# Kernel optimization log

Measured on AMD Instinct MI355X. Metric: run time of the kernel, lower is better.

The kernel has to match this reference:

```python
import jax, jax.numpy as jnp
import numpy as np
import math

B, L, D_MODEL = 4, 2048, 512
EXPAND, D_STATE, D_CONV = 6, 8, 3
D_INNER = EXPAND * D_MODEL            # 3072
DT_RANK = math.ceil(D_MODEL / 16)     # 32
NH = 8
HF = D_MODEL // NH                    # 64


def setup_inputs() -> dict:
    key = jax.random.key(0)
    ks = jax.random.split(key, 16)
    n = lambda k, sh, s=0.02: jax.random.normal(k, sh, dtype=jnp.float32) * s
    return {
        "x": jax.random.normal(ks[0], (B, L, D_MODEL), dtype=jnp.float32),
        "norm_w": jnp.ones((D_MODEL,), jnp.float32),
        "in_proj_w": n(ks[1], (2 * D_INNER, D_MODEL)),
        "conv_w": n(ks[2], (D_INNER, 1, D_CONV), 0.2),
        "conv_b": jnp.zeros((D_INNER,), jnp.float32),
        "x_proj_w": n(ks[3], (DT_RANK + 2 * D_STATE, D_INNER)),
        "dt_head_w": n(ks[4], (D_INNER, DT_RANK)),
        "dt_head_b": jnp.zeros((D_INNER,), jnp.float32),
        "D": jnp.ones((D_INNER,), jnp.float32),
        "reduce_w": n(ks[5], (D_MODEL, D_INNER)),
        "q_net_w": n(ks[6], (D_MODEL, D_MODEL)),
        "gain_q_w": n(ks[7], (D_MODEL, D_MODEL)),
        "gain_k_w": n(ks[8], (D_MODEL, D_MODEL)),
        "alpha": jnp.ones((1,), jnp.float32),
        "beta": jnp.zeros((1,), jnp.float32),
        "qkv_w": n(ks[9], (3 * D_MODEL + NH, D_MODEL)),
        "qkv_b": jnp.zeros((3 * D_MODEL + NH,), jnp.float32),
        "ttt_lr_bias": jnp.zeros((NH,), jnp.float32),
        "W1": n(ks[10], (NH, HF, HF)),
        "b1": jnp.zeros((NH, HF), jnp.float32),
        "token_idx": 1.0 / jnp.arange(1, L + 1, dtype=jnp.float32),
        "token_idx_bias": jnp.zeros((L,), jnp.float32),
        "ttt_ln_w": jnp.ones((NH, HF), jnp.float32),
        "ttt_ln_b": jnp.zeros((NH, HF), jnp.float32),
        "post_norm_w": jnp.ones((D_MODEL,), jnp.float32),
        "post_norm_b": jnp.zeros((D_MODEL,), jnp.float32),
        "wo_w": n(ks[11], (D_MODEL, D_MODEL)),
        "wo_b": jnp.zeros((D_MODEL,), jnp.float32),
    }


def _rmsnorm(x, w, eps=1e-5):
    return x * jax.lax.rsqrt(jnp.mean(x * x, axis=-1, keepdims=True) + eps) * w


def _layernorm(x, w, b, eps=1e-5):
    mu = x.mean(-1, keepdims=True)
    xh = (x - mu) * jax.lax.rsqrt(x.var(-1, keepdims=True) + eps)
    return xh * w + b


def _longhorn_scan(x, z, dt, k, q, dt_b, D):
    # x,z,dt: [B,L,di]; k,q: [B,L,ds].  Online Longhorn recurrence (matches step()).
    def step(s, t):
        x_t, z_t, dt_t, k_t, q_t = t
        dt_t = jax.nn.sigmoid(dt_t + dt_b)
        dt_t = dt_t / (1.0 + dt_t * jnp.sum(k_t * k_t, -1, keepdims=True))
        dB = dt_t[:, :, None] * k_t[:, None, :]                  # [B,di,ds]
        s = s * (1.0 - dB * k_t[:, None, :]) + x_t[:, :, None] * dB
        y_t = jnp.einsum('bdn,bn->bd', s, q_t) + D * x_t
        return s, y_t * jax.nn.silu(z_t)

    s0 = jnp.zeros((x.shape[0], x.shape[2], k.shape[2]), x.dtype)
    xs = tuple(jnp.moveaxis(a, 1, 0) for a in (x, z, dt, k, q))
    _, ys = jax.lax.scan(step, s0, xs)
    return jnp.moveaxis(ys, 0, 1)                                # [B,L,di]


def _ttt(h, qkv_w, qkv_b, ttt_lr_bias, W1, b1, token_idx, token_idx_bias,
         ln_w, ln_b, pn_w, pn_b, wo_w, wo_b, lr_mult=1.0):
    Bh, N, d = h.shape
    proj = h @ qkv_w.T + qkv_b                                   # [B,N,3d+NH]
    XQK, XV, XGate, lr = (proj[..., :d], proj[..., d:2 * d],
                          proj[..., 2 * d:3 * d], proj[..., 3 * d:])

    def heads(a):  # [B,N,d] -> [B*NH,N,HF]
        return a.reshape(Bh, N, NH, HF).transpose(0, 2, 1, 3).reshape(Bh * NH, N, HF)

    XQ = heads(XQK)            # XQ == XK in the source
    XVh = heads(XV)
    ttt_lr = jax.nn.sigmoid(lr + ttt_lr_bias) * lr_mult          # [B,N,NH]
    ttt_lr = jnp.swapaxes(ttt_lr, 0, 1).reshape(N, Bh * NH, 1)   # [N,B*NH,1]
    tok = jnp.maximum(token_idx + token_idx_bias, 0.0)           # [N]

    W1c = jnp.broadcast_to(W1[None], (Bh, NH, HF, HF)).reshape(Bh * NH, HF, HF)
    b1c = jnp.broadcast_to(b1[None], (Bh, NH, HF)).reshape(Bh * NH, HF)
    lnw = jnp.broadcast_to(ln_w[None], (Bh, NH, HF)).reshape(Bh * NH, HF)
    lnb = jnp.broadcast_to(ln_b[None], (Bh, NH, HF)).reshape(Bh * NH, HF)
    eps = 1e-6
    HFf = jnp.float32(HF)

    def step(carry, t):
        W, bb = carry
        xk, xv, lr_t, tok_t = t
        Z1 = jnp.einsum('bf,bfg->bg', xk, W) + bb
        mu = Z1.mean(-1, keepdims=True)
        std = jnp.sqrt(Z1.var(-1, keepdims=True) + eps)
        xh = (Z1 - mu) / std
        # grad of ||LN(Z1) - (XV - XK)||^2 wrt Z1 (ln_fused_l2_bwd)
        go = (lnw * xh + lnb) - (xv - xk)
        gxh = go * lnw
        grad = (HFf * gxh - gxh.sum(-1, keepdims=True)
                - xh * (gxh * xh).sum(-1, keepdims=True)) / (HFf * std)
        eta = lr_t * tok_t                                       # [B*NH,1]
        W = W - eta[:, :, None] * (xk[:, :, None] * grad[:, None, :])
        bb = bb - eta * grad
        Z1q = jnp.einsum('bf,bfg->bg', xk, W) + bb
        mu2 = Z1q.mean(-1, keepdims=True)
        std2 = jnp.sqrt(Z1q.var(-1, keepdims=True) + eps)
        out_t = xk + lnw * (Z1q - mu2) / std2 + lnb
        return (W, bb), out_t

    xs = (jnp.moveaxis(XQ, 1, 0), jnp.moveaxis(XVh, 1, 0), ttt_lr, tok)
    _, ys = jax.lax.scan(step, (W1c, b1c), xs)                   # [N,B*NH,HF]
    xqw = ys.reshape(N, Bh, NH, HF).transpose(1, 0, 2, 3).reshape(Bh, N, d)
    normed = _layernorm(xqw, pn_w, pn_b)
    gated = jax.nn.gelu(XGate, approximate=True) * normed
    return gated @ wo_w.T + wo_b


def reference(x, norm_w, in_proj_w, conv_w, conv_b, x_proj_w, dt_head_w, dt_head_b,
              D, reduce_w, q_net_w, gain_q_w, gain_k_w, alpha, beta,
              qkv_w, qkv_b, ttt_lr_bias, W1, b1, token_idx, token_idx_bias,
              ttt_ln_w, ttt_ln_b, post_norm_w, post_norm_b, wo_w, wo_b):
    residual = x                                   # residual=None in forward
    xn = _rmsnorm(residual, norm_w)
    # ---- Longhorn block ----
    xz = xn @ in_proj_w.T                          # [B,L,2*di]
    xx, z = jnp.split(xz, 2, axis=-1)
    xc = jnp.swapaxes(xx, 1, 2)                    # [B,di,L]
    xc = jax.lax.conv_general_dilated(
        xc, conv_w, (1,), [(D_CONV - 1, 0)],       # causal depthwise conv
        dimension_numbers=('NCH', 'OIH', 'NCH'), feature_group_count=D_INNER)
    xc = jax.nn.silu(xc + conv_b[None, :, None])
    xb = jnp.swapaxes(xc, 1, 2)                    # [B,L,di]
    x_dbl = xb @ x_proj_w.T
    dt = x_dbl[..., :DT_RANK] @ dt_head_w.T        # [B,L,di] (bias added in scan)
    k = x_dbl[..., DT_RANK:DT_RANK + D_STATE]
    q = x_dbl[..., DT_RANK + D_STATE:]
    y = _longhorn_scan(xb, z, dt, k, q, dt_head_b, D)   # h_hidden, [B,L,di]
    # (out_proj output is discarded by PreCoBlock, so not computed)
    h_red = y @ reduce_w.T                          # [B,L,d]
    # ---- TTT corrective branch ----
    c_hidden = _ttt(h_red, qkv_w, qkv_b, ttt_lr_bias, W1, b1, token_idx,
                    token_idx_bias, ttt_ln_w, ttt_ln_b, post_norm_w, post_norm_b,
                    wo_w, wo_b, lr_mult=1.0)
    z_long = h_red @ q_net_w.T
    z_ttt = c_hidden @ q_net_w.T
    gq = h_red @ gain_q_w.T
    gk = h_red @ gain_k_w.T
    # score = mean_i (gq_i . gk_j)/sqrt(d) == (mean_i gq_i) . gk_j / sqrt(d)
    score = jnp.einsum('bd,bld->bl', gq.mean(axis=1), gk) / jnp.sqrt(jnp.float32(D_MODEL))
    gain = jnp.minimum(jax.nn.sigmoid(alpha * score + beta), 0.55)[..., None]
    out = z_long + gain * (z_ttt - z_long)
    return (out, residual, gain)
```

## Files before the change

kernel.cpp:

```cpp
#include <hip/hip_runtime.h>
#include <hip/hip_bf16.h>
#include <cstdint>
#include <cstddef>

#define L_SEQ 2048
#define BATCH 4
#define DM    512
#define DI    3072
#define NROWS (BATCH * L_SEQ)
#define PROJW 1544
#define CTILE 16
#define BDI   (BATCH * DI)
#define SB    64
#define NSB   (L_SEQ / SB)
#define CHT   16
#define LCH   128
#define NLCH  (L_SEQ / LCH)

using bf16 = __hip_bfloat16;

typedef __attribute__((ext_vector_type(8))) short short8v;
typedef __attribute__((ext_vector_type(4))) float f32x4;


__device__ __forceinline__ float sigmoidf_(float x) { return 1.f / (1.f + __expf(-x)); }
__device__ __forceinline__ float us2f(unsigned int u) {
    union { unsigned int i; float f; } c; c.i = u << 16; return c.f;
}
__device__ __forceinline__ bf16  f2b(float f) { return __float2bfloat16(f); }
__device__ __forceinline__ float b2f(bf16 v)  { return __bfloat162float(v); }
__device__ __forceinline__ void st1(float* p, float v) { *p = v; }
__device__ __forceinline__ void st1(bf16* p, float v)  { *p = f2b(v); }

template <int CTRL>
__device__ __forceinline__ float dppadd_(float x) {
    int s = __builtin_amdgcn_update_dpp(0, __builtin_bit_cast(int, x), CTRL, 0xF, 0xF, true);
    return x + __builtin_bit_cast(float, s);
}
__device__ __forceinline__ float wave_sum_u(float x) {
    x = dppadd_<0x111>(x);
    x = dppadd_<0x112>(x);
    x = dppadd_<0x114>(x);
    x = dppadd_<0x118>(x);
    x = dppadd_<0x142>(x);
    x = dppadd_<0x143>(x);
    return __builtin_bit_cast(float,
        __builtin_amdgcn_readlane(__builtin_bit_cast(int, x), 63));
}

__global__ __launch_bounds__(256) void copy4_k(const float4* __restrict__ in,
                                               float4* __restrict__ out, int n) {
    int i = blockIdx.x * 256 + threadIdx.x;
    if (i < n) out[i] = in[i];
}

__global__ __launch_bounds__(256) void cvt_k(const float* __restrict__ in,
                                             bf16* __restrict__ out, int n4) {
    int i = blockIdx.x * 256 + threadIdx.x;
    if (i >= n4) return;
    float4 v = ((const float4*)in)[i];
    out[4 * i + 0] = f2b(v.x);
    out[4 * i + 1] = f2b(v.y);
    out[4 * i + 2] = f2b(v.z);
    out[4 * i + 3] = f2b(v.w);
}

__global__ __launch_bounds__(256) void rmsnorm_k(const float* __restrict__ x,
                                                 const float* __restrict__ w,
                                                 bf16* __restrict__ xn) {
    int r = blockIdx.x, tid = threadIdx.x;
    const float* row = x + (size_t)r * DM;
    float v0 = row[tid], v1 = row[tid + 256];
    float q = v0 * v0 + v1 * v1;
#pragma unroll
    for (int off = 32; off; off >>= 1) q += __shfl_xor(q, off);
    __shared__ float sm[4];
    if ((tid & 63) == 0) sm[tid >> 6] = q;
    __syncthreads();
    q = sm[0] + sm[1] + sm[2] + sm[3];
    float scale = rsqrtf(q * (1.f / 512.f) + 1e-5f);
    bf16* orow = xn + (size_t)r * DM;
    orow[tid]       = f2b(v0 * scale * w[tid]);
    orow[tid + 256] = f2b(v1 * scale * w[tid + 256]);
}

template <int BIAS, typename TC>
__global__ __launch_bounds__(256) void gemm_mfma(const bf16* __restrict__ A, int lda,
                                                 const bf16* __restrict__ Wb, int ldw,
                                                 const float* __restrict__ bias,
                                                 TC* __restrict__ C, int ldc,
                                                 int N, int K) {
    __shared__ __align__(16) bf16 As[128 * 48];
    __shared__ __align__(16) bf16 Ws[128 * 48];
    const int tid = threadIdx.x;
    const int lane = tid & 63;
    const int widx = tid >> 6;
    const int bm = blockIdx.x * 128;
    const int bn = blockIdx.y * 128;
    const int wr = (widx >> 1) * 64;
    const int wc = (widx & 1) * 64;

    f32x4 acc[4][4];
#pragma unroll
    for (int i = 0; i < 4; ++i)
#pragma unroll
        for (int j = 0; j < 4; ++j) acc[i][j] = (f32x4){0.f, 0.f, 0.f, 0.f};

    const int r0 = tid >> 2;
    const int c0 = tid & 3;
    const int frow = lane & 15;
    const int fk = (lane >> 4) * 8;

    int n0 = bn + r0;       if (n0 > N - 1) n0 = N - 1;
    int n1 = bn + r0 + 64;  if (n1 > N - 1) n1 = N - 1;
    const bf16* pa0 = A + (size_t)(bm + r0) * lda + c0 * 8;
    const bf16* pa1 = A + (size_t)(bm + r0 + 64) * lda + c0 * 8;
    const bf16* pb0 = Wb + (size_t)n0 * ldw + c0 * 8;
    const bf16* pb1 = Wb + (size_t)n1 * ldw + c0 * 8;

    for (int k0 = 0; k0 < K; k0 += 32) {
        short8v a0 = *(const short8v*)(pa0 + k0);
        short8v a1 = *(const short8v*)(pa1 + k0);
        short8v b0 = *(const short8v*)(pb0 + k0);
        short8v b1 = *(const short8v*)(pb1 + k0);
        __syncthreads();
        *(short8v*)&As[r0 * 48 + c0 * 8] = a0;
        *(short8v*)&As[(r0 + 64) * 48 + c0 * 8] = a1;
        *(short8v*)&Ws[r0 * 48 + c0 * 8] = b0;
        *(short8v*)&Ws[(r0 + 64) * 48 + c0 * 8] = b1;
        __syncthreads();
        short8v af[4], bg[4];
#pragma unroll
        for (int mi = 0; mi < 4; ++mi)
            af[mi] = *(const short8v*)&As[(wr + mi * 16 + frow) * 48 + fk];
#pragma unroll
        for (int ni = 0; ni < 4; ++ni)
            bg[ni] = *(const short8v*)&Ws[(wc + ni * 16 + frow) * 48 + fk];
#pragma unroll
        for (int mi = 0; mi < 4; ++mi)
#pragma unroll
            for (int ni = 0; ni < 4; ++ni)
                acc[mi][ni] = __builtin_amdgcn_mfma_f32_16x16x32_bf16(
                    af[mi], bg[ni], acc[mi][ni], 0, 0, 0);
    }

#pragma unroll
    for (int ni = 0; ni < 4; ++ni) {
        int col = bn + wc + ni * 16 + (lane & 15);
        if (col < N) {
            float bz = BIAS ? bias[col] : 0.f;
#pragma unroll
            for (int mi = 0; mi < 4; ++mi) {
                int rbase = bm + wr + mi * 16 + (lane >> 4) * 4;
#pragma unroll
                for (int r = 0; r < 4; ++r) {
                    float v = acc[mi][ni][r] + bz;
                    st1(&C[(size_t)(rbase + r) * ldc + col], v);
                }
            }
        }
    }
}

__global__ __launch_bounds__(256) void conv_boundary_k(const bf16* __restrict__ x,
                                                       bf16* __restrict__ side) {
    int idx = blockIdx.x * 256 + threadIdx.x;
    const int total = (L_SEQ / CTILE - 1) * 2 * BDI;
    if (idx >= total) return;
    int col = idx % BDI;
    int rr = idx / BDI;
    int tile = (rr >> 1) + 1;
    int r = rr & 1;
    int b = col / DI, d = col % DI;
    int l = tile * CTILE - 2 + r;
    side[idx] = x[((size_t)b * L_SEQ + l) * DI + d];
}

__global__ __launch_bounds__(256) void conv_tile_k(bf16* __restrict__ x,
                                                   const bf16* __restrict__ side,
                                                   const float* __restrict__ cw,
                                                   const float* __restrict__ cb) {
    int idx = blockIdx.x * 256 + threadIdx.x;
    const int total = (L_SEQ / CTILE) * BDI;
    if (idx >= total) return;
    int col = idx % BDI;
    int tile = idx / BDI;
    int b = col / DI, d = col % DI;
    float w0 = cw[3 * d], w1 = cw[3 * d + 1], w2 = cw[3 * d + 2], bias = cb[d];
    size_t base = ((size_t)b * L_SEQ + tile * CTILE) * DI + d;
    float xm2, xm1;
    if (tile == 0) { xm2 = 0.f; xm1 = 0.f; }
    else {
        const bf16* sp = side + ((size_t)(tile - 1) * 2) * BDI + col;
        xm2 = b2f(sp[0]);
        xm1 = b2f(sp[BDI]);
    }
    float cur = b2f(x[base]);
#pragma unroll
    for (int i = 0; i < CTILE; ++i) {
        float nxt = (i + 1 < CTILE) ? b2f(x[base + (size_t)(i + 1) * DI]) : 0.f;
        float a = bias + w0 * xm2 + w1 * xm1 + w2 * cur;
        x[base + (size_t)i * DI] = f2b(a * sigmoidf_(a));
        xm2 = xm1; xm1 = cur; cur = nxt;
    }
}


__global__ __launch_bounds__(256) void longhorn_p1(const bf16* __restrict__ xb,
                                                   const float* __restrict__ xdbl,
                                                   const float* __restrict__ dtw,
                                                   const float* __restrict__ dtb_v,
                                                   float* __restrict__ pq) {
    int idx = blockIdx.x * 256 + threadIdx.x;
    int ch = idx / BDI;
    int col = idx % BDI;
    int b = col / DI, d = col % DI;
    float w32[32];
#pragma unroll
    for (int i = 0; i < 32; ++i) w32[i] = dtw[d * 32 + i];
    float dtb = dtb_v[d];
    float P[8] = {1.f, 1.f, 1.f, 1.f, 1.f, 1.f, 1.f, 1.f};
    float Q[8] = {0.f, 0.f, 0.f, 0.f, 0.f, 0.f, 0.f, 0.f};
    size_t rbase = ((size_t)b * L_SEQ + ch * LCH) * DI + d;
    const float* xdb = xdbl + ((size_t)b * L_SEQ + ch * LCH) * 48;

    float xv = b2f(xb[rbase]);
    for (int t = 0; t < LCH; ++t) {
        float x_c = xv;
        if (t + 1 < LCH) xv = b2f(xb[rbase + (size_t)(t + 1) * DI]);
        const float* row = xdb + (size_t)t * 48;
        float dt_c = 0.f;
#pragma unroll
        for (int i = 0; i < 32; i += 4) {
            float4 r4 = *(const float4*)(row + i);
            dt_c = fmaf(r4.x, w32[i + 0], dt_c);
            dt_c = fmaf(r4.y, w32[i + 1], dt_c);
            dt_c = fmaf(r4.z, w32[i + 2], dt_c);
            dt_c = fmaf(r4.w, w32[i + 3], dt_c);
        }
        float kq[8];
#pragma unroll
        for (int i = 0; i < 8; i += 4) *(float4*)&kq[i] = *(const float4*)(row + 32 + i);
        float sig = sigmoidf_(dt_c + dtb);
        float ksq = 0.f;
#pragma unroll
        for (int n = 0; n < 8; ++n) ksq = fmaf(kq[n], kq[n], ksq);
        float dts = sig / (1.f + sig * ksq);
#pragma unroll
        for (int n = 0; n < 8; ++n) {
            float dB = dts * kq[n];
            float a = 1.f - dB * kq[n];
            P[n] *= a;
            Q[n] = fmaf(Q[n], a, x_c * dB);
        }
    }
    float* o = pq + (size_t)idx * 16;
#pragma unroll
    for (int n = 0; n < 8; n += 4) {
        *(float4*)(o + n)     = make_float4(P[n], P[n + 1], P[n + 2], P[n + 3]);
        *(float4*)(o + 8 + n) = make_float4(Q[n], Q[n + 1], Q[n + 2], Q[n + 3]);
    }
}

__global__ __launch_bounds__(256) void longhorn_p2(float* __restrict__ pq) {
    int col = blockIdx.x * 256 + threadIdx.x;
    float s[8] = {0.f, 0.f, 0.f, 0.f, 0.f, 0.f, 0.f, 0.f};
    for (int c = 0; c < NLCH; ++c) {
        float* base = pq + ((size_t)c * BDI + col) * 16;
        float P[8], Q[8];
#pragma unroll
        for (int n = 0; n < 8; n += 4) {
            *(float4*)&P[n] = *(const float4*)(base + n);
            *(float4*)&Q[n] = *(const float4*)(base + 8 + n);
        }
#pragma unroll
        for (int n = 0; n < 8; n += 4)
            *(float4*)(base + n) = make_float4(s[n], s[n + 1], s[n + 2], s[n + 3]);
#pragma unroll
        for (int n = 0; n < 8; ++n) s[n] = fmaf(P[n], s[n], Q[n]);
    }
}

__global__ __launch_bounds__(256) void longhorn_p3(bf16* __restrict__ xb_y,
                                                   const bf16* __restrict__ z,
                                                   const float* __restrict__ xdbl,
                                                   const float* __restrict__ dtw,
                                                   const float* __restrict__ dtb_v,
                                                   const float* __restrict__ Dv,
                                                   const float* __restrict__ pq) {
    int idx = blockIdx.x * 256 + threadIdx.x;
    int ch = idx / BDI;
    int col = idx % BDI;
    int b = col / DI, d = col % DI;
    float w32[32];
#pragma unroll
    for (int i = 0; i < 32; ++i) w32[i] = dtw[d * 32 + i];
    float dtb = dtb_v[d], Dd = Dv[d];
    float s[8];
    {
        const float* base = pq + (size_t)idx * 16;
#pragma unroll
        for (int n = 0; n < 8; n += 4) *(float4*)&s[n] = *(const float4*)(base + n);
    }
    size_t rbase = ((size_t)b * L_SEQ + ch * LCH) * DI + d;
    const float* xdb = xdbl + ((size_t)b * L_SEQ + ch * LCH) * 48;

    float xv = b2f(xb_y[rbase]);
    float zv = b2f(z[rbase]);
    for (int t = 0; t < LCH; ++t) {
        float x_c = xv, z_c = zv;
        if (t + 1 < LCH) {
            size_t nidx = rbase + (size_t)(t + 1) * DI;
            xv = b2f(xb_y[nidx]);
            zv = b2f(z[nidx]);
        }
        const float* row = xdb + (size_t)t * 48;
        float dt_c = 0.f;
#pragma unroll
        for (int i = 0; i < 32; i += 4) {
            float4 r4 = *(const float4*)(row + i);
            dt_c = fmaf(r4.x, w32[i + 0], dt_c);
            dt_c = fmaf(r4.y, w32[i + 1], dt_c);
            dt_c = fmaf(r4.z, w32[i + 2], dt_c);
            dt_c = fmaf(r4.w, w32[i + 3], dt_c);
        }
        float kq[16];
#pragma unroll
        for (int i = 0; i < 16; i += 4) *(float4*)&kq[i] = *(const float4*)(row + 32 + i);
        float sig = sigmoidf_(dt_c + dtb);
        float ksq = 0.f;
#pragma unroll
        for (int n = 0; n < 8; ++n) ksq = fmaf(kq[n], kq[n], ksq);
        float dts = sig / (1.f + sig * ksq);
        float y = 0.f;
#pragma unroll
        for (int n = 0; n < 8; ++n) {
            float dB = dts * kq[n];
            s[n] = s[n] * (1.f - dB * kq[n]) + x_c * dB;
            y = fmaf(s[n], kq[8 + n], y);
        }
        y = fmaf(Dd, x_c, y);
        float out = y * (z_c * sigmoidf_(z_c));
        xb_y[rbase + (size_t)t * DI] = f2b(out);
    }
}

__global__ __launch_bounds__(128) void prep_ttt_k(const bf16* __restrict__ proj,
                                                  const float* __restrict__ lr_bias,
                                                  const float* __restrict__ tok_idx,
                                                  const float* __restrict__ tok_bias,
                                                  const float* __restrict__ ln_w,
                                                  const float* __restrict__ ln_b,
                                                  float* __restrict__ xkf,
                                                  float* __restrict__ etav,
                                                  float* __restrict__ q0s) {
    int bh = blockIdx.x >> 4;
    int t = (blockIdx.x & 15) * 128 + threadIdx.x;
    int b = bh >> 3, h = bh & 7;
    const bf16* prow = proj + ((size_t)b * L_SEQ + t) * PROJW;
    const bf16* pk = prow + h * 64;
    const bf16* pv = prow + 512 + h * 64;
    const float* lwp = ln_w + h * 64;
    const float* lbp = ln_b + h * 64;
    float* xo = xkf + ((size_t)bh * L_SEQ + t) * 64;
    float q0 = 0.f;
#pragma unroll
    for (int i = 0; i < 64; i += 8) {
        short8v sk = *(const short8v*)(pk + i);
        short8v sv = *(const short8v*)(pv + i);
        float v[8];
#pragma unroll
        for (int j = 0; j < 8; ++j) {
            float xk = us2f((unsigned short)sk[j]);
            float xv = us2f((unsigned short)sv[j]);
            v[j] = xk;
            q0 = fmaf((lbp[i + j] - xv + xk), lwp[i + j], q0);
        }
        *(float4*)(xo + i)     = make_float4(v[0], v[1], v[2], v[3]);
        *(float4*)(xo + i + 4) = make_float4(v[4], v[5], v[6], v[7]);
    }
    float eta = sigmoidf_(b2f(prow[1536 + h]) + lr_bias[h]) *
                fmaxf(tok_idx[t] + tok_bias[t], 0.f);
    size_t o = (size_t)bh * L_SEQ + t;
    etav[o] = eta;
    q0s[o]  = q0;
}

__global__ __launch_bounds__(64) void gram16_k(const float* __restrict__ xkf,
                                               float* __restrict__ gram) {
    int bh = blockIdx.x >> 7, c16 = blockIdx.x & 127;
    int lane = threadIdx.x;
    __shared__ __align__(16) float xs[16][68];
    const float* src = xkf + ((size_t)bh * L_SEQ + c16 * 16) * 64;
    {
        int r = lane >> 2, cb = (lane & 3) * 16;
#pragma unroll
        for (int j = 0; j < 4; ++j)
            *(float4*)&xs[r][cb + 4 * j] = *(const float4*)(src + (size_t)r * 64 + cb + 4 * j);
    }
    __syncthreads();
    int t = lane >> 2, s0 = lane & 3;
    float* dst = gram + ((size_t)(bh * 128 + c16) * 16 + t) * 16;
#pragma unroll
    for (int jj = 0; jj < 4; ++jj) {
        int s = s0 * 4 + jj;
        float a0 = 0.f, a1 = 0.f, a2 = 0.f, a3 = 0.f;
#pragma unroll
        for (int j = 0; j < 16; ++j) {
            float4 u = *(const float4*)&xs[t][4 * j];
            float4 v = *(const float4*)&xs[s][4 * j];
            a0 = fmaf(u.x, v.x, a0); a1 = fmaf(u.y, v.y, a1);
            a2 = fmaf(u.z, v.z, a2); a3 = fmaf(u.w, v.w, a3);
        }
        dst[s] = (a0 + a1) + (a2 + a3);
    }
}

__global__ __launch_bounds__(64) void ttt_k(const bf16* __restrict__ proj,
                                            const float* __restrict__ xkf,
                                            const float* __restrict__ etav,
                                            const float* __restrict__ q0s,
                                            const float* __restrict__ gram16,
                                            const float* __restrict__ W1,
                                            const float* __restrict__ b1,
                                            const float* __restrict__ ln_w,
                                            const float* __restrict__ ln_b,
                                            bf16* __restrict__ xqw) {
    const int lane = threadIdx.x;
    const int bh = blockIdx.x;
    const int b = bh >> 3, h = bh & 7;

    __shared__ __align__(16) float xkb[2][SB][64];
    __shared__ __align__(16) bf16  xvb[2][SB][64];
    __shared__ __align__(16) float kb[2][4][CHT][CHT];
    __shared__ __align__(16) float sc[2][2][SB];
    __shared__ __align__(16) float zbb[CHT][64];
    __shared__ __align__(16) float z1qb[CHT][64];
    __shared__ __align__(16) float egb[CHT][64];
    __shared__ float mub[CHT];

    float W[64];
#pragma unroll
    for (int f = 0; f < 64; ++f) W[f] = W1[(size_t)(h * 64 + f) * 64 + lane];
    float bvec = b1[h * 64 + lane];
    float lw = ln_w[h * 64 + lane];
    float lb = ln_b[h * 64 + lane];
    float p = lw * lw;

    const float* kfg = xkf + (size_t)bh * L_SEQ * 64;
    const bf16*  pvg = proj + (size_t)b * L_SEQ * PROJW + 512 + h * 64;
    const float* evg = etav + (size_t)bh * L_SEQ;
    const float* qg  = q0s + (size_t)bh * L_SEQ;
    const float* gmg = gram16 + (size_t)bh * 128 * 256;

    auto stage_async = [&](int c, int bi) {
        const int t0g = c * SB;
#pragma unroll
        for (int i = 0; i < 16; ++i) {
            const float* gp = kfg + (size_t)(t0g + 4 * i) * 64 + lane * 4;
            __builtin_amdgcn_global_load_lds(
                (const __attribute__((address_space(1))) void*)gp,
                (__attribute__((address_space(3))) void*)&xkb[bi][4 * i][0], 16, 0, 0);
        }
#pragma unroll
        for (int i = 0; i < 8; ++i) {
            const bf16* gp = pvg + (size_t)(t0g + 8 * i + (lane >> 3)) * PROJW + (lane & 7) * 8;
            __builtin_amdgcn_global_load_lds(
                (const __attribute__((address_space(1))) void*)gp,
                (__attribute__((address_space(3))) void*)&xvb[bi][8 * i][0], 16, 0, 0);
        }
#pragma unroll
        for (int i = 0; i < 4; ++i) {
            const float* gp = gmg + (size_t)c * 1024 + i * 256 + lane * 4;
            __builtin_amdgcn_global_load_lds(
                (const __attribute__((address_space(1))) void*)gp,
                (__attribute__((address_space(3))) void*)(&kb[bi][0][0][0] + i * 256), 16, 0, 0);
        }
        {
            const float* g0 = evg + t0g + lane;
            __builtin_amdgcn_global_load_lds(
                (const __attribute__((address_space(1))) void*)g0,
                (__attribute__((address_space(3))) void*)&sc[bi][0][0], 4, 0, 0);
            const float* g1 = qg + t0g + lane;
            __builtin_amdgcn_global_load_lds(
                (const __attribute__((address_space(1))) void*)g1,
                (__attribute__((address_space(3))) void*)&sc[bi][1][0], 4, 0, 0);
        }
    };
    auto matvec16 = [&](int nbuf, int nt0) {
        for (int t = 0; t < CHT; ++t) {
            const float4* row = (const float4*)&xkb[nbuf][nt0 + t][0];
            float a0 = 0.f, a1 = 0.f, a2 = 0.f, a3 = 0.f;
#pragma unroll
            for (int j = 0; j < 16; ++j) {
                float4 kv = row[j];
                a0 = fmaf(kv.x, W[4 * j + 0], a0);
                a1 = fmaf(kv.y, W[4 * j + 1], a1);
                a2 = fmaf(kv.z, W[4 * j + 2], a2);
                a3 = fmaf(kv.w, W[4 * j + 3], a3);
            }
            float zb = (a0 + a1) + (a2 + a3) + bvec;
            zbb[t][lane] = zb;
            float m = wave_sum_u(zb) * 0.015625f;
            if (lane == 0) mub[t] = m;
        }
    };

    stage_async(0, 0);
    asm volatile("s_waitcnt vmcnt(0)" ::: "memory");
    __builtin_amdgcn_sched_barrier(0);
    matvec16(0, 0);

    bf16* xq = xqw + ((size_t)b * L_SEQ) * DM + h * 64 + lane;

    for (int c = 0; c < NSB; ++c) {
        const int cur = c & 1;
        if (c + 1 < NSB) stage_async(c + 1, 1 - cur);
#pragma unroll 1
        for (int sub = 0; sub < 4; ++sub) {
            const int t0 = sub * CHT;
            float eg[CHT];
            float bacc = 0.f;
#pragma unroll
            for (int t = 0; t < CHT; ++t) {
                float kr[CHT];
                const float4* krow = (const float4*)&kb[cur][sub][t][0];
                *(float4*)&kr[0]  = krow[0];
                *(float4*)&kr[4]  = krow[1];
                *(float4*)&kr[8]  = krow[2];
                *(float4*)&kr[12] = krow[3];
                float zb_v = zbb[t][lane];
                float xk_c = xkb[cur][t0 + t][lane];
                float xv_c = b2f(xvb[cur][t0 + t][lane]);
                float eta  = sc[cur][0][t0 + t];
                float q0u  = sc[cur][1][t0 + t];
                float muv  = mub[t];

                float gg0 = bacc, gg1 = 0.f, gg2 = 0.f, gg3 = 0.f;
#pragma unroll
                for (int s = 0; s < t; ++s) {
                    if ((s & 3) == 0) gg0 = fmaf(kr[s], eg[s], gg0);
                    else if ((s & 3) == 1) gg1 = fmaf(kr[s], eg[s], gg1);
                    else if ((s & 3) == 2) gg2 = fmaf(kr[s], eg[s], gg2);
                    else gg3 = fmaf(kr[s], eg[s], gg3);
                }
                float z1 = zb_v - ((gg0 + gg1) + (gg2 + gg3));
                float d = z1 - muv;
                float q = (lb - xv_c + xk_c) * lw;
                float S2  = wave_sum_u(d * d);
                float PZ1 = wave_sum_u(p * d);
                float PZ2 = wave_sum_u(p * d * d);
                float Q1  = wave_sum_u(q * d);
                float istd = rsqrtf(S2 * 0.015625f + 1e-6f);
                float A_ = fmaf(istd, PZ1, q0u);
                float Bv = fmaf(istd * istd, PZ2, istd * Q1);
                float xh = d * istd;
                float gxh = fmaf(p, xh, q);
                float grad = (64.f * gxh - A_ - xh * Bv) * (istd * 0.015625f);
                float egt = eta * grad;
                eg[t] = egt;
                egb[t][lane] = egt;
                z1qb[t][lane] = fmaf(-eta * (kr[t] + 1.f), grad, z1);
                bacc += egt;
            }
            for (int t = 0; t < CHT; ++t) {
                float dq = z1qb[t][lane] - mub[t];
                float SQ = wave_sum_u(dq * dq);
                float istd2 = rsqrtf(SQ * 0.015625f + 1e-6f);
                float xk_c = xkb[cur][t0 + t][lane];
                float outv = fmaf(lw, dq * istd2, xk_c + lb);
                xq[(size_t)(c * SB + t0 + t) * DM] = f2b(outv);
            }
            bool last = (c == NSB - 1) && (sub == 3);
            if (!last) {
                for (int s = 0; s < CHT; ++s) {
                    float egs = egb[s][lane];
                    const float4* row = (const float4*)&xkb[cur][t0 + s][0];
#pragma unroll
                    for (int j = 0; j < 16; ++j) {
                        float4 kv = row[j];
                        W[4 * j + 0] = fmaf(-egs, kv.x, W[4 * j + 0]);
                        W[4 * j + 1] = fmaf(-egs, kv.y, W[4 * j + 1]);
                        W[4 * j + 2] = fmaf(-egs, kv.z, W[4 * j + 2]);
                        W[4 * j + 3] = fmaf(-egs, kv.w, W[4 * j + 3]);
                    }
                }
                bvec -= bacc;
                int nbuf = cur, nt0 = t0 + CHT;
                if (sub == 3) {
                    nbuf = 1 - cur; nt0 = 0;
                    asm volatile("s_waitcnt vmcnt(0)" ::: "memory");
                    __builtin_amdgcn_sched_barrier(0);
                }
                matvec16(nbuf, nt0);
            }
        }
    }
}

__global__ __launch_bounds__(256) void gated_k(const bf16* __restrict__ xqw,
                                               const bf16* __restrict__ proj,
                                               const float* __restrict__ pnw,
                                               const float* __restrict__ pnb,
                                               bf16* __restrict__ gated) {
    int r = blockIdx.x, tid = threadIdx.x;
    const bf16* row = xqw + (size_t)r * DM;
    float v0 = b2f(row[tid]), v1 = b2f(row[tid + 256]);
    float s = v0 + v1, q = v0 * v0 + v1 * v1;
#pragma unroll
    for (int off = 32; off; off >>= 1) {
        s += __shfl_xor(s, off);
        q += __shfl_xor(q, off);
    }
    __shared__ float sm[8];
    if ((tid & 63) == 0) { sm[tid >> 6] = s; sm[4 + (tid >> 6)] = q; }
    __syncthreads();
    s = sm[0] + sm[1] + sm[2] + sm[3];
    q = sm[4] + sm[5] + sm[6] + sm[7];
    float mu = s * (1.f / 512.f);
    float var = q * (1.f / 512.f) - mu * mu;
    float istd = rsqrtf(var + 1e-5f);
    const bf16* grow = proj + (size_t)r * PROJW + 1024;
    bf16* orow = gated + (size_t)r * DM;
#pragma unroll
    for (int e = 0; e < 2; ++e) {
        int c = tid + e * 256;
        float xv = (e == 0) ? v0 : v1;
        float nv = (xv - mu) * istd * pnw[c] + pnb[c];
        float g = b2f(grow[c]);
        float gg = 0.5f * g * (1.f + tanhf(0.7978845608028654f * (g + 0.044715f * g * g * g)));
        orow[c] = f2b(gg * nv);
    }
}

__global__ __launch_bounds__(256) void mean1_k(const float* __restrict__ gq,
                                               float* __restrict__ partial) {
    int blk = blockIdx.x;
    int b = blk >> 4, c = blk & 15;
    int tid = threadIdx.x;
    const float* p = gq + ((size_t)b * L_SEQ + c * 128) * DM + tid * 2;
    float a0 = 0.f, a1 = 0.f;
    for (int l = 0; l < 128; ++l) {
        float2 v = *(const float2*)(p + (size_t)l * DM);
        a0 += v.x; a1 += v.y;
    }
    partial[(size_t)blk * DM + tid * 2]     = a0;
    partial[(size_t)blk * DM + tid * 2 + 1] = a1;
}
__global__ __launch_bounds__(256) void mean2_k(const float* __restrict__ partial,
                                               float* __restrict__ gqm) {
    int t = blockIdx.x * 256 + threadIdx.x;
    if (t >= 2048) return;
    int b = t >> 9, d = t & 511;
    float acc = 0.f;
#pragma unroll
    for (int c = 0; c < 16; ++c) acc += partial[(size_t)(b * 16 + c) * DM + d];
    gqm[t] = acc * (1.f / 2048.f);
}

__global__ __launch_bounds__(64) void final_k(const float* __restrict__ zl,
                                              const float* __restrict__ zt,
                                              const float* __restrict__ gk,
                                              const float* __restrict__ gqm,
                                              const float* __restrict__ alpha,
                                              const float* __restrict__ beta,
                                              float* __restrict__ out,
                                              float* __restrict__ gain_out) {
    int r = blockIdx.x;
    int lane = threadIdx.x;
    int b = r >> 11;
    const float* gkr = gk + (size_t)r * DM;
    const float* gmb = gqm + b * DM;
    float acc = 0.f;
#pragma unroll
    for (int i = 0; i < 8; ++i) acc = fmaf(gmb[lane + 64 * i], gkr[lane + 64 * i], acc);
#pragma unroll
    for (int off = 32; off; off >>= 1) acc += __shfl_xor(acc, off);
    float score = acc * 0.04419417382415922f;
    float g = sigmoidf_(alpha[0] * score + beta[0]);
    g = fminf(g, 0.55f);
    if (lane == 0) gain_out[r] = g;
    const float* zlr = zl + (size_t)r * DM;
    const float* ztr = zt + (size_t)r * DM;
    float* orow = out + (size_t)r * DM;
#pragma unroll
    for (int i = 0; i < 8; ++i) {
        int c = lane + 64 * i;
        float a = zlr[c];
        orow[c] = a + g * (ztr[c] - a);
    }
}


extern "C" void kernel_launch(void* const* d_in, const int* in_sizes, int n_in,
                              void* d_out, int out_size, void* d_ws, size_t ws_size,
                              hipStream_t stream) {
    const float* x           = (const float*)d_in[0];
    const float* norm_w      = (const float*)d_in[1];
    const float* in_proj_w   = (const float*)d_in[2];
    const float* conv_w      = (const float*)d_in[3];
    const float* conv_b      = (const float*)d_in[4];
    const float* x_proj_w    = (const float*)d_in[5];
    const float* dt_head_w   = (const float*)d_in[6];
    const float* dt_head_b   = (const float*)d_in[7];
    const float* Dvec        = (const float*)d_in[8];
    const float* reduce_w    = (const float*)d_in[9];
    const float* q_net_w     = (const float*)d_in[10];
    const float* gain_q_w    = (const float*)d_in[11];
    const float* gain_k_w    = (const float*)d_in[12];
    const float* alpha       = (const float*)d_in[13];
    const float* beta        = (const float*)d_in[14];
    const float* qkv_w       = (const float*)d_in[15];
    const float* qkv_b       = (const float*)d_in[16];
    const float* ttt_lr_bias = (const float*)d_in[17];
    const float* W1          = (const float*)d_in[18];
    const float* b1          = (const float*)d_in[19];
    const float* token_idx   = (const float*)d_in[20];
    const float* token_bias  = (const float*)d_in[21];
    const float* ttt_ln_w    = (const float*)d_in[22];
    const float* ttt_ln_b    = (const float*)d_in[23];
    const float* post_norm_w = (const float*)d_in[24];
    const float* post_norm_b = (const float*)d_in[25];
    const float* wo_w        = (const float*)d_in[26];
    const float* wo_b        = (const float*)d_in[27];

    const size_t SZ_ROWDM = (size_t)NROWS * DM;
    const size_t MB = 1024u * 1024u;
    char* base = (char*)d_ws;

    float* out_p  = (float*)d_out;
    float* res_p  = out_p + SZ_ROWDM;
    float* gain_p = out_p + 2 * SZ_ROWDM;

    copy4_k<<<(int)(SZ_ROWDM / 4 / 256), 256, 0, stream>>>(
        (const float4*)x, (float4*)res_p, (int)(SZ_ROWDM / 4));

    if (ws_size < 116 * MB) return;

    bf16*  ws0   = (bf16*)base;
    bf16*  xn    = (bf16*)(base + 7 * MB);
    bf16*  h_red = xn;
    bf16*  cside = (bf16*)(base + 7 * MB);
    float* lpq   = (float*)base;
    bf16*  bufX  = (bf16*)(base + 16 * MB);
    bf16*  bufZ  = (bf16*)(base + 64 * MB);
    float* xdbl  = (float*)(base + 112 * MB);
    float* gqm   = (float*)(base + 113 * MB + 512 * 1024);
    float* mpart = (float*)(base + 114 * MB);
    bf16*  proj  = bufX;
    bf16*  xqw   = bufZ;
    bf16*  gated = (bf16*)(base + 72 * MB);
    bf16*  chid  = (bf16*)(base + 80 * MB);
    float* gramb = (float*)(base + 88 * MB);
    float* zlong = (float*)(base + 88 * MB);
    float* xkf   = (float*)(base + 42 * MB);
    float* etav  = (float*)(base + 58 * MB);
    float* q0s   = (float*)(base + 58 * MB + 512 * 1024);
    float* zttt  = (float*)(base + 42 * MB);
    float* gq    = (float*)(base + 16 * MB);
    float* gk    = (float*)(base + 64 * MB);

    rmsnorm_k<<<NROWS, 256, 0, stream>>>(x, norm_w, xn);

    cvt_k<<<(2 * DI * DM / 4 + 255) / 256, 256, 0, stream>>>(in_proj_w, ws0, 2 * DI * DM / 4);
    {
        dim3 g(NROWS / 128, DI / 128);
        gemm_mfma<0, bf16><<<g, 256, 0, stream>>>(xn, DM, ws0, DM, nullptr, bufX, DI, DI, DM);
        gemm_mfma<0, bf16><<<g, 256, 0, stream>>>(xn, DM, ws0 + (size_t)DI * DM, DM, nullptr, bufZ, DI, DI, DM);
    }

    conv_boundary_k<<<((L_SEQ / CTILE - 1) * 2 * BDI) / 256, 256, 0, stream>>>(bufX, cside);
    conv_tile_k<<<((L_SEQ / CTILE) * BDI) / 256, 256, 0, stream>>>(bufX, cside, conv_w, conv_b);

    cvt_k<<<(48 * DI / 4 + 255) / 256, 256, 0, stream>>>(x_proj_w, ws0, 48 * DI / 4);
    {
        dim3 g(NROWS / 128, 1);
        gemm_mfma<0, float><<<g, 256, 0, stream>>>(bufX, DI, ws0, DI, nullptr, xdbl, 48, 48, DI);
    }

    longhorn_p1<<<(NLCH * BDI) / 256, 256, 0, stream>>>(bufX, xdbl, dt_head_w, dt_head_b, lpq);
    longhorn_p2<<<BDI / 256, 256, 0, stream>>>(lpq);
    longhorn_p3<<<(NLCH * BDI) / 256, 256, 0, stream>>>(bufX, bufZ, xdbl, dt_head_w,
                                                        dt_head_b, Dvec, lpq);

    cvt_k<<<(DM * DI / 4 + 255) / 256, 256, 0, stream>>>(reduce_w, ws0, DM * DI / 4);
    {
        dim3 g(NROWS / 128, DM / 128);
        gemm_mfma<0, bf16><<<g, 256, 0, stream>>>(bufX, DI, ws0, DI, nullptr, h_red, DM, DM, DI);
    }

    cvt_k<<<(PROJW * DM / 4 + 255) / 256, 256, 0, stream>>>(qkv_w, ws0, PROJW * DM / 4);
    {
        dim3 g(NROWS / 128, (PROJW + 127) / 128);
        gemm_mfma<1, bf16><<<g, 256, 0, stream>>>(h_red, DM, ws0, DM, qkv_b, proj, PROJW, PROJW, DM);
    }

    prep_ttt_k<<<32 * 16, 128, 0, stream>>>(proj, ttt_lr_bias, token_idx, token_bias,
                                            ttt_ln_w, ttt_ln_b, xkf, etav, q0s);
    gram16_k<<<32 * 128, 64, 0, stream>>>(xkf, gramb);
    ttt_k<<<BATCH * 8, 64, 0, stream>>>(proj, xkf, etav, q0s, gramb, W1, b1,
                                        ttt_ln_w, ttt_ln_b, xqw);

    gated_k<<<NROWS, 256, 0, stream>>>(xqw, proj, post_norm_w, post_norm_b, gated);

    cvt_k<<<(DM * DM / 4 + 255) / 256, 256, 0, stream>>>(wo_w, ws0, DM * DM / 4);
    {
        dim3 g(NROWS / 128, DM / 128);
        gemm_mfma<1, bf16><<<g, 256, 0, stream>>>(gated, DM, ws0, DM, wo_b, chid, DM, DM, DM);
    }

    cvt_k<<<(DM * DM / 4 + 255) / 256, 256, 0, stream>>>(q_net_w, ws0, DM * DM / 4);
    {
        dim3 g(NROWS / 128, DM / 128);
        gemm_mfma<0, float><<<g, 256, 0, stream>>>(h_red, DM, ws0, DM, nullptr, zlong, DM, DM, DM);
        gemm_mfma<0, float><<<g, 256, 0, stream>>>(chid, DM, ws0, DM, nullptr, zttt, DM, DM, DM);
    }

    cvt_k<<<(DM * DM / 4 + 255) / 256, 256, 0, stream>>>(gain_q_w, ws0, DM * DM / 4);
    {
        dim3 g(NROWS / 128, DM / 128);
        gemm_mfma<0, float><<<g, 256, 0, stream>>>(h_red, DM, ws0, DM, nullptr, gq, DM, DM, DM);
    }
    cvt_k<<<(DM * DM / 4 + 255) / 256, 256, 0, stream>>>(gain_k_w, ws0, DM * DM / 4);
    {
        dim3 g(NROWS / 128, DM / 128);
        gemm_mfma<0, float><<<g, 256, 0, stream>>>(h_red, DM, ws0, DM, nullptr, gk, DM, DM, DM);
    }

    mean1_k<<<64, 256, 0, stream>>>(gq, mpart);
    mean2_k<<<8, 256, 0, stream>>>(mpart, gqm);
    final_k<<<NROWS, 64, 0, stream>>>(zlong, zttt, gk, gqm, alpha, beta, out_p, gain_p);
}
```

Baseline: 2.472 ms.

## Process two batch-head TTT sequences per wavefront to interleave serial chains

The sequential TTT kernel now gives each 64-lane block two (batch, head) streams instead of one, halving the grid to 16 blocks. Every stage (staging loads, matvec, per-token gradient, output, W update) is duplicated across the two streams so their independent dependency chains and wave reductions can interleave. This hides latency in a kernel bound by its serial chain. In exchange it doubles register pressure (two 64-float W arrays) and LDS use, and uses only 16 of the many CUs.

```diff
diff --git a/kernel.cpp b/kernel.cpp
--- a/kernel.cpp
+++ b/kernel.cpp
@@ -204,7 +204,6 @@
         xm2 = xm1; xm1 = cur; cur = nxt;
     }
 }
-
 
 __global__ __launch_bounds__(256) void longhorn_p1(const bf16* __restrict__ xb,
                                                    const float* __restrict__ xdbl,
@@ -427,82 +426,101 @@
                                             const float* __restrict__ ln_b,
                                             bf16* __restrict__ xqw) {
     const int lane = threadIdx.x;
-    const int bh = blockIdx.x;
-    const int b = bh >> 3, h = bh & 7;
-
-    __shared__ __align__(16) float xkb[2][SB][64];
-    __shared__ __align__(16) bf16  xvb[2][SB][64];
-    __shared__ __align__(16) float kb[2][4][CHT][CHT];
-    __shared__ __align__(16) float sc[2][2][SB];
-    __shared__ __align__(16) float zbb[CHT][64];
-    __shared__ __align__(16) float z1qb[CHT][64];
-    __shared__ __align__(16) float egb[CHT][64];
-    __shared__ float mub[CHT];
-
-    float W[64];
-#pragma unroll
-    for (int f = 0; f < 64; ++f) W[f] = W1[(size_t)(h * 64 + f) * 64 + lane];
-    float bvec = b1[h * 64 + lane];
-    float lw = ln_w[h * 64 + lane];
-    float lb = ln_b[h * 64 + lane];
-    float p = lw * lw;
-
-    const float* kfg = xkf + (size_t)bh * L_SEQ * 64;
-    const bf16*  pvg = proj + (size_t)b * L_SEQ * PROJW + 512 + h * 64;
-    const float* evg = etav + (size_t)bh * L_SEQ;
-    const float* qg  = q0s + (size_t)bh * L_SEQ;
-    const float* gmg = gram16 + (size_t)bh * 128 * 256;
+    const int blk = blockIdx.x;
+
+    __shared__ __align__(16) float xkb[2][2][SB][64];
+    __shared__ __align__(16) bf16  xvb[2][2][SB][64];
+    __shared__ __align__(16) float kb[2][2][4][CHT][CHT];
+    __shared__ __align__(16) float etab[2][2][SB];
+    __shared__ __align__(16) float q0b[2][2][SB];
+    __shared__ __align__(16) float zbb[2][CHT][64];
+    __shared__ __align__(16) float z1qb[2][CHT][64];
+    __shared__ __align__(16) float egb[2][CHT][64];
+    __shared__ float mub[2][CHT];
+
+    float W[2][64];
+    float bvec[2], lw[2], lb[2], p[2];
+    const float* kfg[2];
+    const bf16*  pvg[2];
+    const float* evg[2];
+    const float* qg[2];
+    const float* gmg[2];
+    bf16* xq[2];
+
+#pragma unroll
+    for (int q = 0; q < 2; ++q) {
+        int bh = 2 * blk + q;
+        int b = bh >> 3, h = bh & 7;
+#pragma unroll
+        for (int f = 0; f < 64; ++f) W[q][f] = W1[(size_t)(h * 64 + f) * 64 + lane];
+        bvec[q] = b1[h * 64 + lane];
+        lw[q] = ln_w[h * 64 + lane];
+        lb[q] = ln_b[h * 64 + lane];
+        p[q] = lw[q] * lw[q];
+        kfg[q] = xkf + (size_t)bh * L_SEQ * 64;
+        pvg[q] = proj + (size_t)b * L_SEQ * PROJW + 512 + h * 64;
+        evg[q] = etav + (size_t)bh * L_SEQ;
+        qg[q]  = q0s + (size_t)bh * L_SEQ;
+        gmg[q] = gram16 + (size_t)bh * 128 * 256;
+        xq[q]  = xqw + ((size_t)b * L_SEQ) * DM + h * 64 + lane;
+    }
 
     auto stage_async = [&](int c, int bi) {
         const int t0g = c * SB;
 #pragma unroll
-        for (int i = 0; i < 16; ++i) {
-            const float* gp = kfg + (size_t)(t0g + 4 * i) * 64 + lane * 4;
-            __builtin_amdgcn_global_load_lds(
-                (const __attribute__((address_space(1))) void*)gp,
-                (__attribute__((address_space(3))) void*)&xkb[bi][4 * i][0], 16, 0, 0);
-        }
-#pragma unroll
-        for (int i = 0; i < 8; ++i) {
-            const bf16* gp = pvg + (size_t)(t0g + 8 * i + (lane >> 3)) * PROJW + (lane & 7) * 8;
-            __builtin_amdgcn_global_load_lds(
-                (const __attribute__((address_space(1))) void*)gp,
-                (__attribute__((address_space(3))) void*)&xvb[bi][8 * i][0], 16, 0, 0);
-        }
-#pragma unroll
-        for (int i = 0; i < 4; ++i) {
-            const float* gp = gmg + (size_t)c * 1024 + i * 256 + lane * 4;
-            __builtin_amdgcn_global_load_lds(
-                (const __attribute__((address_space(1))) void*)gp,
-                (__attribute__((address_space(3))) void*)(&kb[bi][0][0][0] + i * 256), 16, 0, 0);
-        }
-        {
-            const float* g0 = evg + t0g + lane;
-            __builtin_amdgcn_global_load_lds(
-                (const __attribute__((address_space(1))) void*)g0,
-                (__attribute__((address_space(3))) void*)&sc[bi][0][0], 4, 0, 0);
-            const float* g1 = qg + t0g + lane;
-            __builtin_amdgcn_global_load_lds(
-                (const __attribute__((address_space(1))) void*)g1,
-                (__attribute__((address_space(3))) void*)&sc[bi][1][0], 4, 0, 0);
+        for (int q = 0; q < 2; ++q) {
+#pragma unroll
+            for (int i = 0; i < 16; ++i) {
+                const float* gp = kfg[q] + (size_t)(t0g + 4 * i) * 64 + lane * 4;
+                __builtin_amdgcn_global_load_lds(
+                    (const __attribute__((address_space(1))) void*)gp,
+                    (__attribute__((address_space(3))) void*)&xkb[q][bi][4 * i][0], 16, 0, 0);
+            }
+#pragma unroll
+            for (int i = 0; i < 8; ++i) {
+                const bf16* gp = pvg[q] + (size_t)(t0g + 8 * i + (lane >> 3)) * PROJW + (lane & 7) * 8;
+                __builtin_amdgcn_global_load_lds(
+                    (const __attribute__((address_space(1))) void*)gp,
+                    (__attribute__((address_space(3))) void*)&xvb[q][bi][8 * i][0], 16, 0, 0);
+            }
+#pragma unroll
+            for (int i = 0; i < 4; ++i) {
+                const float* gp = gmg[q] + (size_t)c * 1024 + i * 256 + lane * 4;
+                __builtin_amdgcn_global_load_lds(
+                    (const __attribute__((address_space(1))) void*)gp,
+                    (__attribute__((address_space(3))) void*)(&kb[q][bi][0][0][0] + i * 256), 16, 0, 0);
+            }
+            {
+                const float* g0 = evg[q] + t0g + lane;
+                __builtin_amdgcn_global_load_lds(
+                    (const __attribute__((address_space(1))) void*)g0,
+                    (__attribute__((address_space(3))) void*)&etab[q][bi][0], 4, 0, 0);
+                const float* g1 = qg[q] + t0g + lane;
+                __builtin_amdgcn_global_load_lds(
+                    (const __attribute__((address_space(1))) void*)g1,
+                    (__attribute__((address_space(3))) void*)&q0b[q][bi][0], 4, 0, 0);
+            }
         }
     };
     auto matvec16 = [&](int nbuf, int nt0) {
         for (int t = 0; t < CHT; ++t) {
-            const float4* row = (const float4*)&xkb[nbuf][nt0 + t][0];
-            float a0 = 0.f, a1 = 0.f, a2 = 0.f, a3 = 0.f;
-#pragma unroll
-            for (int j = 0; j < 16; ++j) {
-                float4 kv = row[j];
-                a0 = fmaf(kv.x, W[4 * j + 0], a0);
-                a1 = fmaf(kv.y, W[4 * j + 1], a1);
-                a2 = fmaf(kv.z, W[4 * j + 2], a2);
-                a3 = fmaf(kv.w, W[4 * j + 3], a3);
+#pragma unroll
+            for (int q = 0; q < 2; ++q) {
+                const float4* row = (const float4*)&xkb[q][nbuf][nt0 + t][0];
+                float a0 = 0.f, a1 = 0.f, a2 = 0.f, a3 = 0.f;
+#pragma unroll
+                for (int j = 0; j < 16; ++j) {
+                    float4 kv = row[j];
+                    a0 = fmaf(kv.x, W[q][4 * j + 0], a0);
+                    a1 = fmaf(kv.y, W[q][4 * j + 1], a1);
+                    a2 = fmaf(kv.z, W[q][4 * j + 2], a2);
+                    a3 = fmaf(kv.w, W[q][4 * j + 3], a3);
+                }
+                float zb = (a0 + a1) + (a2 + a3) + bvec[q];
+                zbb[q][t][lane] = zb;
+                float m = wave_sum_u(zb) * 0.015625f;
+                if (lane == 0) mub[q][t] = m;
             }
-            float zb = (a0 + a1) + (a2 + a3) + bvec;
-            zbb[t][lane] = zb;
-            float m = wave_sum_u(zb) * 0.015625f;
-            if (lane == 0) mub[t] = m;
         }
     };
 
@@ -510,8 +528,6 @@
     asm volatile("s_waitcnt vmcnt(0)" ::: "memory");
     __builtin_amdgcn_sched_barrier(0);
     matvec16(0, 0);
-
-    bf16* xq = xqw + ((size_t)b * L_SEQ) * DM + h * 64 + lane;
 
     for (int c = 0; c < NSB; ++c) {
         const int cur = c & 1;
@@ -519,73 +535,83 @@
 #pragma unroll 1
         for (int sub = 0; sub < 4; ++sub) {
             const int t0 = sub * CHT;
-            float eg[CHT];
-            float bacc = 0.f;
+            float eg[2][CHT];
+            float bacc[2] = {0.f, 0.f};
 #pragma unroll
             for (int t = 0; t < CHT; ++t) {
-                float kr[CHT];
-                const float4* krow = (const float4*)&kb[cur][sub][t][0];
-                *(float4*)&kr[0]  = krow[0];
-                *(float4*)&kr[4]  = krow[1];
-                *(float4*)&kr[8]  = krow[2];
-                *(float4*)&kr[12] = krow[3];
-                float zb_v = zbb[t][lane];
-                float xk_c = xkb[cur][t0 + t][lane];
-                float xv_c = b2f(xvb[cur][t0 + t][lane]);
-                float eta  = sc[cur][0][t0 + t];
-                float q0u  = sc[cur][1][t0 + t];
-                float muv  = mub[t];
-
-                float gg0 = bacc, gg1 = 0.f, gg2 = 0.f, gg3 = 0.f;
-#pragma unroll
-                for (int s = 0; s < t; ++s) {
-                    if ((s & 3) == 0) gg0 = fmaf(kr[s], eg[s], gg0);
-                    else if ((s & 3) == 1) gg1 = fmaf(kr[s], eg[s], gg1);
-                    else if ((s & 3) == 2) gg2 = fmaf(kr[s], eg[s], gg2);
-                    else gg3 = fmaf(kr[s], eg[s], gg3);
+#pragma unroll
+                for (int q = 0; q < 2; ++q) {
+                    float kr[CHT];
+                    const float4* krow = (const float4*)&kb[q][cur][sub][t][0];
+                    *(float4*)&kr[0]  = krow[0];
+                    *(float4*)&kr[4]  = krow[1];
+                    *(float4*)&kr[8]  = krow[2];
+                    *(float4*)&kr[12] = krow[3];
+                    float zb_v = zbb[q][t][lane];
+                    float xk_c = xkb[q][cur][t0 + t][lane];
+                    float xv_c = b2f(xvb[q][cur][t0 + t][lane]);
+                    float eta  = etab[q][cur][t0 + t];
+                    float q0u  = q0b[q][cur][t0 + t];
+                    float muv  = mub[q][t];
+
+                    float gg0 = bacc[q], gg1 = 0.f, gg2 = 0.f, gg3 = 0.f;
+#pragma unroll
+                    for (int s = 0; s < t; ++s) {
+                        if ((s & 3) == 0) gg0 = fmaf(kr[s], eg[q][s], gg0);
+                        else if ((s & 3) == 1) gg1 = fmaf(kr[s], eg[q][s], gg1);
+                        else if ((s & 3) == 2) gg2 = fmaf(kr[s], eg[q][s], gg2);
+                        else gg3 = fmaf(kr[s], eg[q][s], gg3);
+                    }
+                    float z1 = zb_v - ((gg0 + gg1) + (gg2 + gg3));
+                    float d = z1 - muv;
+                    float qv = (lb[q] - xv_c + xk_c) * lw[q];
+                    float S2  = wave_sum_u(d * d);
+                    float PZ1 = wave_sum_u(p[q] * d);
+                    float PZ2 = wave_sum_u(p[q] * d * d);
+                    float Q1  = wave_sum_u(qv * d);
+                    float istd = rsqrtf(S2 * 0.015625f + 1e-6f);
+                    float A_ = fmaf(istd, PZ1, q0u);
+                    float Bv = fmaf(istd * istd, PZ2, istd * Q1);
+                    float xh = d * istd;
+                    float gxh = fmaf(p[q], xh, qv);
+                    float grad = (64.f * gxh - A_ - xh * Bv) * (istd * 0.015625f);
+                    float egt = eta * grad;
+                    eg[q][t] = egt;
+                    egb[q][t][lane] = egt;
+                    z1qb[q][t][lane] = fmaf(-eta * (kr[t] + 1.f), grad, z1);
+                    bacc[q] += egt;
                 }
-                float z1 = zb_v - ((gg0 + gg1) + (gg2 + gg3));
-                float d = z1 - muv;
-                float q = (lb - xv_c + xk_c) * lw;
-                float S2  = wave_sum_u(d * d);
-                float PZ1 = wave_sum_u(p * d);
-                float PZ2 = wave_sum_u(p * d * d);
-                float Q1  = wave_sum_u(q * d);
-                float istd = rsqrtf(S2 * 0.015625f + 1e-6f);
-                float A_ = fmaf(istd, PZ1, q0u);
-                float Bv = fmaf(istd * istd, PZ2, istd * Q1);
-                float xh = d * istd;
-                float gxh = fmaf(p, xh, q);
-                float grad = (64.f * gxh - A_ - xh * Bv) * (istd * 0.015625f);
-                float egt = eta * grad;
-                eg[t] = egt;
-                egb[t][lane] = egt;
-                z1qb[t][lane] = fmaf(-eta * (kr[t] + 1.f), grad, z1);
-                bacc += egt;
             }
             for (int t = 0; t < CHT; ++t) {
-                float dq = z1qb[t][lane] - mub[t];
-                float SQ = wave_sum_u(dq * dq);
-                float istd2 = rsqrtf(SQ * 0.015625f + 1e-6f);
-                float xk_c = xkb[cur][t0 + t][lane];
-                float outv = fmaf(lw, dq * istd2, xk_c + lb);
-                xq[(size_t)(c * SB + t0 + t) * DM] = f2b(outv);
+#pragma unroll
+                for (int q = 0; q < 2; ++q) {
+                    float dq = z1qb[q][t][lane] - mub[q][t];
+                    float SQ = wave_sum_u(dq * dq);
+                    float istd2 = rsqrtf(SQ * 0.015625f + 1e-6f);
+                    float xk_c = xkb[q][cur][t0 + t][lane];
+                    float outv = fmaf(lw[q], dq * istd2, xk_c + lb[q]);
+                    xq[q][(size_t)(c * SB + t0 + t) * DM] = f2b(outv);
+                }
             }
             bool last = (c == NSB - 1) && (sub == 3);
             if (!last) {
                 for (int s = 0; s < CHT; ++s) {
-                    float egs = egb[s][lane];
-                    const float4* row = (const float4*)&xkb[cur][t0 + s][0];
-#pragma unroll
-                    for (int j = 0; j < 16; ++j) {
-                        float4 kv = row[j];
-                        W[4 * j + 0] = fmaf(-egs, kv.x, W[4 * j + 0]);
-                        W[4 * j + 1] = fmaf(-egs, kv.y, W[4 * j + 1]);
-                        W[4 * j + 2] = fmaf(-egs, kv.z, W[4 * j + 2]);
-                        W[4 * j + 3] = fmaf(-egs, kv.w, W[4 * j + 3]);
+#pragma unroll
+                    for (int q = 0; q < 2; ++q) {
+                        float egs = egb[q][s][lane];
+                        const float4* row = (const float4*)&xkb[q][cur][t0 + s][0];
+#pragma unroll
+                        for (int j = 0; j < 16; ++j) {
+                            float4 kv = row[j];
+                            W[q][4 * j + 0] = fmaf(-egs, kv.x, W[q][4 * j + 0]);
+                            W[q][4 * j + 1] = fmaf(-egs, kv.y, W[q][4 * j + 1]);
+                            W[q][4 * j + 2] = fmaf(-egs, kv.z, W[q][4 * j + 2]);
+                            W[q][4 * j + 3] = fmaf(-egs, kv.w, W[q][4 * j + 3]);
+                        }
                     }
                 }
-                bvec -= bacc;
+#pragma unroll
+                for (int q = 0; q < 2; ++q) bvec[q] -= bacc[q];
                 int nbuf = cur, nt0 = t0 + CHT;
                 if (sub == 3) {
                     nbuf = 1 - cur; nt0 = 0;
@@ -798,8 +824,8 @@
     prep_ttt_k<<<32 * 16, 128, 0, stream>>>(proj, ttt_lr_bias, token_idx, token_bias,
                                             ttt_ln_w, ttt_ln_b, xkf, etav, q0s);
     gram16_k<<<32 * 128, 64, 0, stream>>>(xkf, gramb);
-    ttt_k<<<BATCH * 8, 64, 0, stream>>>(proj, xkf, etav, q0s, gramb, W1, b1,
-                                        ttt_ln_w, ttt_ln_b, xqw);
+    ttt_k<<<16, 64, 0, stream>>>(proj, xkf, etav, q0s, gramb, W1, b1,
+                                 ttt_ln_w, ttt_ln_b, xqw);
 
     gated_k<<<NROWS, 256, 0, stream>>>(xqw, proj, post_norm_w, post_norm_b, gated);
 
```

After: 5.851 ms. +136.7%, slower.
